# Optimization experiments

Hardware: AMD Instinct MI355X
Metric: run time of the kernel (lower is better)

## Reference

```python
import jax, jax.numpy as jnp
import numpy as np

B, H, N, DK, DV = 2, 8, 2048, 64, 64

def setup_inputs() -> dict:
    key = jax.random.key(0)
    k1, k2, k3, k4 = jax.random.split(key, 4)
    q = jax.random.normal(k1, (B, H, N, DK), dtype=jnp.float32)
    k = jax.random.normal(k2, (B, H, N, DK), dtype=jnp.float32)
    v = jax.random.normal(k3, (B, H, N, DV), dtype=jnp.float32)
    # decay mask, strictly positive in (0,1)
    omask = jax.random.uniform(k4, (B, H, N, N), dtype=jnp.float32, minval=1e-3, maxval=1.0)
    return {"q": q, "k": k, "v": v, "omask": omask}

def reference(q, k, v, omask):
    # coefficients from the decay mask
    q_bar_coef = omask[..., :, 0] / jnp.sqrt(omask.sum(axis=-1))  # (B,H,n)
    k_bar_coef = 1.0 / omask[..., :, 0]                            # (B,H,n)
    q_bar = q_bar_coef[..., None] * q                               # (B,H,n,dk)
    k_bar = k_bar_coef[..., None] * k                               # (B,H,n,dk)
    # normalizer P (detached in original)
    T = jnp.cumsum(k_bar, axis=-2)                                  # (B,H,n,dk)
    P = jnp.einsum('bhia,bhia->bhi', T, q_bar)                      # (B,H,n)
    P = jnp.maximum(jnp.abs(jax.lax.stop_gradient(P)), 1.0)[..., None]
    # cumulative outer-product state D: (B,H,n,dk,dv)
    D = jnp.cumsum(jnp.einsum('bhia,bhic->bhiac', k_bar, v), axis=-3)
    O = jnp.einsum('bhia,bhiac->bhic', q_bar, D) / P                # (B,H,n,dv)
    return O
```

## Files before the change

kernel.cpp:

```cpp
#include <hip/hip_runtime.h>
#include <cmath>

constexpr int B_ = 2, H_ = 8, N_ = 2048, DK_ = 64, DV_ = 64;
constexpr int BH_ = B_ * H_;
constexpr int C_ = 64;
constexpr int NC_ = N_ / C_;
constexpr int NCH_ = BH_ * NC_;
constexpr int SCAN_BLOCKS = (BH_ * ((DK_ * DV_) / 4 + DK_ / 4)) / 256;

using f32x16 = __attribute__((ext_vector_type(16))) float;
using bf16x8 = __attribute__((ext_vector_type(8))) __bf16;

__device__ inline unsigned short bfr(float x) {
  unsigned u = __float_as_uint(x);
  return (unsigned short)((u + 0x7FFFu + ((u >> 16) & 1u)) >> 16);
}
__device__ inline unsigned pk2(float lo, float hi) {
  return (unsigned)bfr(lo) | ((unsigned)bfr(hi) << 16);
}
__device__ inline int swi(int row, int a) {
  return (row * 128 + (((a * 2) ^ ((row & 7) << 4)))) >> 1;
}

__global__ __launch_bounds__(256) void chunksum_kernel(const float* __restrict__ kg,
                                                       const float* __restrict__ vg,
                                                       const float* __restrict__ om,
                                                       float* __restrict__ ksum,
                                                       float* __restrict__ kvsum) {
  __shared__ float kb[C_][DK_];
  __shared__ float vs[C_][DV_];
  __shared__ float smkc[C_];
  int chunk = blockIdx.x;
  int bh = chunk / NC_, ci = chunk - bh * NC_;
  int r0 = ci * C_;
  int rowb = bh * N_ + r0;
  size_t gbase = (size_t)rowb * DK_;
  int t = threadIdx.x;
  if (t < 64) smkc[t] = 1.0f / om[(size_t)(rowb + t) * N_];
  __syncthreads();
#pragma unroll
  for (int p = 0; p < 4; ++p) {
    int f = t + p * 256;
    int row = f >> 4, col = (f & 15) * 4;
    float sc = smkc[row];
    float4 k4 = *(const float4*)(kg + gbase + (size_t)f * 4);
    k4.x *= sc; k4.y *= sc; k4.z *= sc; k4.w *= sc;
    *(float4*)&kb[row][col] = k4;
    *(float4*)&vs[row][col] = *(const float4*)(vg + gbase + (size_t)f * 4);
  }
  __syncthreads();
  int dk0 = (t & 15) * 4, dv0 = (t >> 4) * 4;
  float acc[4][4] = {};
  float ks[4] = {};
  for (int r = 0; r < C_; ++r) {
    float4 k4 = *(const float4*)&kb[r][dk0];
    float4 v4 = *(const float4*)&vs[r][dv0];
    float ka[4] = {k4.x, k4.y, k4.z, k4.w};
    float va[4] = {v4.x, v4.y, v4.z, v4.w};
#pragma unroll
    for (int i = 0; i < 4; ++i) {
      ks[i] += ka[i];
#pragma unroll
      for (int j = 0; j < 4; ++j) acc[i][j] += ka[i] * va[j];
    }
  }
  float* kvc = kvsum + (size_t)chunk * (DK_ * DV_);
#pragma unroll
  for (int i = 0; i < 4; ++i)
    *(float4*)(kvc + (size_t)(dk0 + i) * DV_ + dv0) =
        make_float4(acc[i][0], acc[i][1], acc[i][2], acc[i][3]);
  if (t < 16) {
#pragma unroll
    for (int i = 0; i < 4; ++i) ksum[(size_t)chunk * DK_ + dk0 + i] = ks[i];
  }
}

__global__ __launch_bounds__(256) void coef_scan_kernel(const float* __restrict__ om,
                                                        float* __restrict__ qc,
                                                        float* __restrict__ kc,
                                                        float* __restrict__ ksum,
                                                        float* __restrict__ kvsum) {
  int t = threadIdx.x;
  if (blockIdx.x < SCAN_BLOCKS) {
    constexpr int PER4 = (DK_ * DV_) / 4 + DK_ / 4;
    int idx = blockIdx.x * 256 + t;
    int bh = idx / PER4, e = idx - bh * PER4;
    float4* p;
    size_t stride;
    if (e < (DK_ * DV_) / 4) {
      p = (float4*)(kvsum + (size_t)bh * NC_ * (DK_ * DV_)) + e;
      stride = (DK_ * DV_) / 4;
    } else {
      p = (float4*)(ksum + (size_t)bh * NC_ * DK_) + (e - (DK_ * DV_) / 4);
      stride = DK_ / 4;
    }
    float4 run = make_float4(0.f, 0.f, 0.f, 0.f);
    float4 buf[8];
    for (int b = 0; b < NC_ / 8; ++b) {
#pragma unroll
      for (int u = 0; u < 8; ++u) buf[u] = p[(size_t)(b * 8 + u) * stride];
#pragma unroll
      for (int u = 0; u < 8; ++u) {
        p[(size_t)(b * 8 + u) * stride] = run;
        run.x += buf[u].x; run.y += buf[u].y;
        run.z += buf[u].z; run.w += buf[u].w;
      }
    }
  } else {
    int row = (blockIdx.x - SCAN_BLOCKS) * 4 + (t >> 6);
    int lane = t & 63;
    const float* r = om + (size_t)row * N_;
    float s = 0.f;
#pragma unroll
    for (int kk = 0; kk < N_ / 256; ++kk) {
      float4 v4 = *(const float4*)(r + kk * 256 + lane * 4);
      s += (v4.x + v4.y) + (v4.z + v4.w);
    }
#pragma unroll
    for (int off = 32; off > 0; off >>= 1) s += __shfl_xor(s, off, 64);
    if (lane == 0) {
      float o0 = r[0];
      qc[row] = o0 / sqrtf(s);
      kc[row] = 1.0f / o0;
    }
  }
}

__global__ __launch_bounds__(256) void out_mfma_kernel(
    const float* __restrict__ qg, const float* __restrict__ kg,
    const float* __restrict__ vg, const float* __restrict__ qc,
    const float* __restrict__ kc, const float* __restrict__ ksum,
    const float* __restrict__ kvsum, float* __restrict__ outg) {
  __shared__ unsigned short qb[64 * 64];
  __shared__ unsigned short kb[64 * 64];
  __shared__ unsigned short sS[64 * 64];
  __shared__ unsigned short vT[64 * 64];
  __shared__ unsigned short dT[64 * 64];
  __shared__ float Tc[2][64][68];
  __shared__ float Tl[64];
  __shared__ float Pf[64];

  const int chunk = blockIdx.x;
  const int bh = chunk >> 5, ci = chunk & 31;
  const int r0 = ci * C_;
  const int rowb = bh * N_ + r0;
  const size_t gbase = (size_t)rowb * DK_;
  const int t = threadIdx.x;
  const int i = t >> 2, a0 = (t & 3) * 16;

  float xq[16];
  {
    float qcv = qc[rowb + i];
    float kcv = kc[rowb + i];
    float xk[16], xv[16], xd[16];
    {
      const float* qp = qg + gbase + (size_t)i * 64 + a0;
      const float* kp = kg + gbase + (size_t)i * 64 + a0;
      const float* vp = vg + gbase + (size_t)i * 64 + a0;
      const float* dp = kvsum + (size_t)chunk * (DK_ * DV_) + (size_t)i * 64 + a0;
#pragma unroll
      for (int u = 0; u < 4; ++u) {
        *(float4*)&xq[u * 4] = *(const float4*)(qp + u * 4);
        *(float4*)&xk[u * 4] = *(const float4*)(kp + u * 4);
        *(float4*)&xv[u * 4] = *(const float4*)(vp + u * 4);
        *(float4*)&xd[u * 4] = *(const float4*)(dp + u * 4);
      }
    }
#pragma unroll
    for (int u = 0; u < 16; ++u) { xq[u] *= qcv; xk[u] *= kcv; }
#pragma unroll
    for (int u4 = 0; u4 < 4; ++u4)
      *(float4*)&Tc[0][i][a0 + u4 * 4] = *(const float4*)&xk[u4 * 4];
    unsigned* qbu = (unsigned*)qb;
    unsigned* kbu = (unsigned*)kb;
#pragma unroll
    for (int u = 0; u < 8; ++u) {
      int a = a0 + 2 * u;
      int bi = (i * 128 + (((a * 2) ^ ((i & 7) << 4)))) >> 2;
      qbu[bi] = pk2(xq[2 * u], xq[2 * u + 1]);
      kbu[bi] = pk2(xk[2 * u], xk[2 * u + 1]);
    }
#pragma unroll
    for (int u = 0; u < 16; ++u) {
      int c = a0 + u;
      vT[swi(c, i)] = bfr(xv[u]);
      dT[swi(c, i)] = bfr(xd[u]);
    }
    if (t < 64) Tl[t] = ksum[(size_t)chunk * DK_ + t];
  }
  __syncthreads();
  {
    int p = 0;
#pragma unroll
    for (int step = 1; step < 64; step <<= 1) {
      float4 cur[4], prv[4];
#pragma unroll
      for (int u4 = 0; u4 < 4; ++u4) {
        cur[u4] = *(const float4*)&Tc[p][i][a0 + u4 * 4];
        if (i >= step)
          prv[u4] = *(const float4*)&Tc[p][i - step][a0 + u4 * 4];
        else
          prv[u4] = make_float4(0.f, 0.f, 0.f, 0.f);
      }
#pragma unroll
      for (int u4 = 0; u4 < 4; ++u4) {
        float4 w = make_float4(cur[u4].x + prv[u4].x, cur[u4].y + prv[u4].y,
                               cur[u4].z + prv[u4].z, cur[u4].w + prv[u4].w);
        *(float4*)&Tc[p ^ 1][i][a0 + u4 * 4] = w;
      }
      __syncthreads();
      p ^= 1;
    }
  }
  {
    float part = 0.f;
#pragma unroll
    for (int u = 0; u < 16; ++u)
      part += xq[u] * (Tl[a0 + u] + Tc[0][i][a0 + u]);
    part += __shfl_xor(part, 1, 64);
    part += __shfl_xor(part, 2, 64);
    if ((t & 3) == 0) Pf[i] = 1.0f / fmaxf(fabsf(part), 1.0f);
  }
  const int lane = t & 63, w = t >> 6;
  const int wr = w >> 1, wc = w & 1;
  const int half = lane >> 5, col = lane & 31;
  const int arow = 32 * wr + col;
  const int bcol = 32 * wc + col;
  f32x16 accS;
#pragma unroll
  for (int r = 0; r < 16; ++r) accS[r] = 0.f;
#pragma unroll
  for (int kk = 0; kk < 4; ++kk) {
    int aa = kk * 16 + half * 8;
    bf16x8 af = *(const bf16x8*)&qb[swi(arow, aa)];
    bf16x8 bf = *(const bf16x8*)&kb[swi(bcol, aa)];
    accS = __builtin_amdgcn_mfma_f32_32x32x16_bf16(af, bf, accS, 0, 0, 0);
  }
#pragma unroll
  for (int r = 0; r < 16; ++r) {
    int iloc = (r & 3) + 8 * (r >> 2) + 4 * half;
    int ii = 32 * wr + iloc;
    int jj = 32 * wc + col;
    float m = (jj <= ii) ? accS[r] : 0.f;
    sS[swi(ii, jj)] = bfr(m);
  }
  __syncthreads();
  f32x16 acc;
#pragma unroll
  for (int r = 0; r < 16; ++r) acc[r] = 0.f;
#pragma unroll
  for (int kk = 0; kk < 4; ++kk) {
    int j0 = kk * 16 + half * 8;
    bf16x8 af = *(const bf16x8*)&sS[swi(arow, j0)];
    bf16x8 bf = *(const bf16x8*)&vT[swi(bcol, j0)];
    acc = __builtin_amdgcn_mfma_f32_32x32x16_bf16(af, bf, acc, 0, 0, 0);
  }
#pragma unroll
  for (int kk = 0; kk < 4; ++kk) {
    int aa = kk * 16 + half * 8;
    bf16x8 af = *(const bf16x8*)&qb[swi(arow, aa)];
    bf16x8 bf = *(const bf16x8*)&dT[swi(bcol, aa)];
    acc = __builtin_amdgcn_mfma_f32_32x32x16_bf16(af, bf, acc, 0, 0, 0);
  }
  float* ob = outg + (size_t)rowb * DV_;
#pragma unroll
  for (int r = 0; r < 16; ++r) {
    int iloc = (r & 3) + 8 * (r >> 2) + 4 * half;
    int ii = 32 * wr + iloc;
    int cc = 32 * wc + col;
    ob[(size_t)ii * DV_ + cc] = acc[r] * Pf[ii];
  }
}

extern "C" void kernel_launch(void* const* d_in, const int* in_sizes, int n_in,
                              void* d_out, int out_size, void* d_ws, size_t ws_size,
                              hipStream_t stream) {
  const float* q = (const float*)d_in[0];
  const float* k = (const float*)d_in[1];
  const float* v = (const float*)d_in[2];
  const float* om = (const float*)d_in[3];
  float* out = (float*)d_out;

  float* ws = (float*)d_ws;
  float* qc = ws;
  float* kc = qc + BH_ * N_;
  float* ksum = kc + BH_ * N_;
  float* kv = ksum + (size_t)NCH_ * DK_;

  chunksum_kernel<<<NCH_, 256, 0, stream>>>(k, v, om, ksum, kv);
  coef_scan_kernel<<<SCAN_BLOCKS + BH_ * N_ / 4, 256, 0, stream>>>(om, qc, kc,
                                                                   ksum, kv);
  out_mfma_kernel<<<NCH_, 256, 0, stream>>>(q, k, v, qc, kc, ksum, kv, out);
}
```

Before: 69.01 us.

## Fuse chunk-sum and coefficient kernels, compute prefix sums inside output kernel

Merges the per-chunk k/kv summation with the mask row-sum coefficient computation into one launch. It drops the separate cross-chunk scan pass: each output block now sums all earlier chunk kv states and k sums directly while loading its inputs. This saves one launch and the scan's read-modify-write of the state buffer. In exchange, later chunks read up to 31 prior 16KB states, so the output kernel does more memory traffic and its load is skewed toward later chunks. V is also stored as bf16 in shared memory in the front kernel, which lowers precision there.

```diff
diff --git a/kernel.cpp b/kernel.cpp
--- a/kernel.cpp
+++ b/kernel.cpp
@@ -6,7 +6,6 @@
 constexpr int C_ = 64;
 constexpr int NC_ = N_ / C_;
 constexpr int NCH_ = BH_ * NC_;
-constexpr int SCAN_BLOCKS = (BH_ * ((DK_ * DV_) / 4 + DK_ / 4)) / 256;
 
 using f32x16 = __attribute__((ext_vector_type(16))) float;
 using bf16x8 = __attribute__((ext_vector_type(8))) __bf16;
@@ -18,96 +17,71 @@
 __device__ inline unsigned pk2(float lo, float hi) {
   return (unsigned)bfr(lo) | ((unsigned)bfr(hi) << 16);
 }
+__device__ inline float bf2f(unsigned short s) {
+  return __uint_as_float(((unsigned)s) << 16);
+}
 __device__ inline int swi(int row, int a) {
   return (row * 128 + (((a * 2) ^ ((row & 7) << 4)))) >> 1;
 }
 
-__global__ __launch_bounds__(256) void chunksum_kernel(const float* __restrict__ kg,
-                                                       const float* __restrict__ vg,
-                                                       const float* __restrict__ om,
-                                                       float* __restrict__ ksum,
-                                                       float* __restrict__ kvsum) {
+__global__ __launch_bounds__(256) void front_kernel(const float* __restrict__ kg,
+                                                    const float* __restrict__ vg,
+                                                    const float* __restrict__ om,
+                                                    float* __restrict__ qc,
+                                                    float* __restrict__ kc,
+                                                    float* __restrict__ ksum,
+                                                    float* __restrict__ kvsum) {
   __shared__ float kb[C_][DK_];
-  __shared__ float vs[C_][DV_];
+  __shared__ unsigned short vsb[C_][DV_];
   __shared__ float smkc[C_];
-  int chunk = blockIdx.x;
-  int bh = chunk / NC_, ci = chunk - bh * NC_;
-  int r0 = ci * C_;
-  int rowb = bh * N_ + r0;
-  size_t gbase = (size_t)rowb * DK_;
   int t = threadIdx.x;
-  if (t < 64) smkc[t] = 1.0f / om[(size_t)(rowb + t) * N_];
-  __syncthreads();
-#pragma unroll
-  for (int p = 0; p < 4; ++p) {
-    int f = t + p * 256;
-    int row = f >> 4, col = (f & 15) * 4;
-    float sc = smkc[row];
-    float4 k4 = *(const float4*)(kg + gbase + (size_t)f * 4);
-    k4.x *= sc; k4.y *= sc; k4.z *= sc; k4.w *= sc;
-    *(float4*)&kb[row][col] = k4;
-    *(float4*)&vs[row][col] = *(const float4*)(vg + gbase + (size_t)f * 4);
-  }
-  __syncthreads();
-  int dk0 = (t & 15) * 4, dv0 = (t >> 4) * 4;
-  float acc[4][4] = {};
-  float ks[4] = {};
-  for (int r = 0; r < C_; ++r) {
-    float4 k4 = *(const float4*)&kb[r][dk0];
-    float4 v4 = *(const float4*)&vs[r][dv0];
-    float ka[4] = {k4.x, k4.y, k4.z, k4.w};
-    float va[4] = {v4.x, v4.y, v4.z, v4.w};
-#pragma unroll
-    for (int i = 0; i < 4; ++i) {
-      ks[i] += ka[i];
-#pragma unroll
-      for (int j = 0; j < 4; ++j) acc[i][j] += ka[i] * va[j];
-    }
-  }
-  float* kvc = kvsum + (size_t)chunk * (DK_ * DV_);
-#pragma unroll
-  for (int i = 0; i < 4; ++i)
-    *(float4*)(kvc + (size_t)(dk0 + i) * DV_ + dv0) =
-        make_float4(acc[i][0], acc[i][1], acc[i][2], acc[i][3]);
-  if (t < 16) {
-#pragma unroll
-    for (int i = 0; i < 4; ++i) ksum[(size_t)chunk * DK_ + dk0 + i] = ks[i];
-  }
-}
-
-__global__ __launch_bounds__(256) void coef_scan_kernel(const float* __restrict__ om,
-                                                        float* __restrict__ qc,
-                                                        float* __restrict__ kc,
-                                                        float* __restrict__ ksum,
-                                                        float* __restrict__ kvsum) {
-  int t = threadIdx.x;
-  if (blockIdx.x < SCAN_BLOCKS) {
-    constexpr int PER4 = (DK_ * DV_) / 4 + DK_ / 4;
-    int idx = blockIdx.x * 256 + t;
-    int bh = idx / PER4, e = idx - bh * PER4;
-    float4* p;
-    size_t stride;
-    if (e < (DK_ * DV_) / 4) {
-      p = (float4*)(kvsum + (size_t)bh * NC_ * (DK_ * DV_)) + e;
-      stride = (DK_ * DV_) / 4;
-    } else {
-      p = (float4*)(ksum + (size_t)bh * NC_ * DK_) + (e - (DK_ * DV_) / 4);
-      stride = DK_ / 4;
-    }
-    float4 run = make_float4(0.f, 0.f, 0.f, 0.f);
-    float4 buf[8];
-    for (int b = 0; b < NC_ / 8; ++b) {
-#pragma unroll
-      for (int u = 0; u < 8; ++u) buf[u] = p[(size_t)(b * 8 + u) * stride];
-#pragma unroll
-      for (int u = 0; u < 8; ++u) {
-        p[(size_t)(b * 8 + u) * stride] = run;
-        run.x += buf[u].x; run.y += buf[u].y;
-        run.z += buf[u].z; run.w += buf[u].w;
-      }
+  if (blockIdx.x < NCH_) {
+    int chunk = blockIdx.x;
+    int bh = chunk / NC_, ci = chunk - bh * NC_;
+    int r0 = ci * C_;
+    int rowb = bh * N_ + r0;
+    size_t gbase = (size_t)rowb * DK_;
+    if (t < 64) smkc[t] = 1.0f / om[(size_t)(rowb + t) * N_];
+    __syncthreads();
+#pragma unroll
+    for (int p = 0; p < 4; ++p) {
+      int f = t + p * 256;
+      int row = f >> 4, col = (f & 15) * 4;
+      float sc = smkc[row];
+      float4 k4 = *(const float4*)(kg + gbase + (size_t)f * 4);
+      k4.x *= sc; k4.y *= sc; k4.z *= sc; k4.w *= sc;
+      *(float4*)&kb[row][col] = k4;
+      float4 v4 = *(const float4*)(vg + gbase + (size_t)f * 4);
+      vsb[row][col + 0] = bfr(v4.x); vsb[row][col + 1] = bfr(v4.y);
+      vsb[row][col + 2] = bfr(v4.z); vsb[row][col + 3] = bfr(v4.w);
+    }
+    __syncthreads();
+    int dk0 = (t & 15) * 4, dv0 = (t >> 4) * 4;
+    float acc[4][4] = {};
+    float ks[4] = {};
+    for (int r = 0; r < C_; ++r) {
+      float4 k4 = *(const float4*)&kb[r][dk0];
+      ushort4 vu = *(const ushort4*)&vsb[r][dv0];
+      float ka[4] = {k4.x, k4.y, k4.z, k4.w};
+      float va[4] = {bf2f(vu.x), bf2f(vu.y), bf2f(vu.z), bf2f(vu.w)};
+#pragma unroll
+      for (int i = 0; i < 4; ++i) {
+        ks[i] += ka[i];
+#pragma unroll
+        for (int j = 0; j < 4; ++j) acc[i][j] += ka[i] * va[j];
+      }
+    }
+    float* kvc = kvsum + (size_t)chunk * (DK_ * DV_);
+#pragma unroll
+    for (int i = 0; i < 4; ++i)
+      *(float4*)(kvc + (size_t)(dk0 + i) * DV_ + dv0) =
+          make_float4(acc[i][0], acc[i][1], acc[i][2], acc[i][3]);
+    if (t < 16) {
+#pragma unroll
+      for (int i = 0; i < 4; ++i) ksum[(size_t)chunk * DK_ + dk0 + i] = ks[i];
     }
   } else {
-    int row = (blockIdx.x - SCAN_BLOCKS) * 4 + (t >> 6);
+    int row = (blockIdx.x - NCH_) * 4 + (t >> 6);
     int lane = t & 63;
     const float* r = om + (size_t)row * N_;
     float s = 0.f;
@@ -148,22 +122,43 @@
   const int t = threadIdx.x;
   const int i = t >> 2, a0 = (t & 3) * 16;
 
+  float pre[16];
+#pragma unroll
+  for (int u = 0; u < 16; ++u) pre[u] = 0.f;
+  {
+    const float* kvb = kvsum + (size_t)(bh * NC_) * (DK_ * DV_)
+                       + (size_t)i * 64 + a0;
+    for (int cc = 0; cc < ci; ++cc) {
+      const float* pp2 = kvb + (size_t)cc * (DK_ * DV_);
+#pragma unroll
+      for (int u4 = 0; u4 < 4; ++u4) {
+        float4 x = *(const float4*)(pp2 + u4 * 4);
+        pre[u4 * 4 + 0] += x.x; pre[u4 * 4 + 1] += x.y;
+        pre[u4 * 4 + 2] += x.z; pre[u4 * 4 + 3] += x.w;
+      }
+    }
+    if (t < 64) {
+      float s = 0.f;
+      const float* ksb = ksum + (size_t)(bh * NC_) * DK_ + t;
+      for (int cc = 0; cc < ci; ++cc) s += ksb[(size_t)cc * DK_];
+      Tl[t] = s;
+    }
+  }
+
   float xq[16];
   {
     float qcv = qc[rowb + i];
     float kcv = kc[rowb + i];
-    float xk[16], xv[16], xd[16];
+    float xk[16], xv[16];
     {
       const float* qp = qg + gbase + (size_t)i * 64 + a0;
       const float* kp = kg + gbase + (size_t)i * 64 + a0;
       const float* vp = vg + gbase + (size_t)i * 64 + a0;
-      const float* dp = kvsum + (size_t)chunk * (DK_ * DV_) + (size_t)i * 64 + a0;
 #pragma unroll
       for (int u = 0; u < 4; ++u) {
         *(float4*)&xq[u * 4] = *(const float4*)(qp + u * 4);
         *(float4*)&xk[u * 4] = *(const float4*)(kp + u * 4);
         *(float4*)&xv[u * 4] = *(const float4*)(vp + u * 4);
-        *(float4*)&xd[u * 4] = *(const float4*)(dp + u * 4);
       }
     }
 #pragma unroll
@@ -184,9 +179,8 @@
     for (int u = 0; u < 16; ++u) {
       int c = a0 + u;
       vT[swi(c, i)] = bfr(xv[u]);
-      dT[swi(c, i)] = bfr(xd[u]);
-    }
-    if (t < 64) Tl[t] = ksum[(size_t)chunk * DK_ + t];
+      dT[swi(c, i)] = bfr(pre[u]);
+    }
   }
   __syncthreads();
   {
@@ -287,8 +281,7 @@
   float* ksum = kc + BH_ * N_;
   float* kv = ksum + (size_t)NCH_ * DK_;
 
-  chunksum_kernel<<<NCH_, 256, 0, stream>>>(k, v, om, ksum, kv);
-  coef_scan_kernel<<<SCAN_BLOCKS + BH_ * N_ / 4, 256, 0, stream>>>(om, qc, kc,
-                                                                   ksum, kv);
+  front_kernel<<<NCH_ + BH_ * N_ / 4, 256, 0, stream>>>(k, v, om, qc, kc,
+                                                        ksum, kv);
   out_mfma_kernel<<<NCH_, 256, 0, stream>>>(q, k, v, qc, kc, ksum, kv, out);
 }
```

Result: slower. 79.16 us (+14.7%).
